# Kernel optimization log

Hardware: AMD Instinct MI355X
Metric: run time of the kernel (lower is better)

## Reference

```python
import jax, jax.numpy as jnp
import numpy as np

N, E, G, D = 100000, 1600000, 1000, 32
EPS = 1e-5


def setup_inputs() -> dict:
    key = jax.random.key(0)
    ks = jax.random.split(key, 24)
    inp = {
        'h': jax.random.normal(ks[0], (N, D), dtype=jnp.float32),
        'src': jax.random.randint(ks[1], (E,), 0, N, dtype=jnp.int32),
        'dst': jax.random.randint(ks[2], (E,), 0, N, dtype=jnp.int32),
        'graph_id': jnp.sort(jax.random.randint(ks[3], (N,), 0, G, dtype=jnp.int32)),
    }
    dims = [D, 32, 32, 32, 1]
    ki = 4
    for i in range(4):
        inp[f'conv_w{i}'] = jax.random.normal(ks[ki], (dims[i], dims[i + 1]), dtype=jnp.float32) * 0.1; ki += 1
        inp[f'conv_b{i}'] = jax.random.normal(ks[ki], (dims[i + 1],), dtype=jnp.float32) * 0.1; ki += 1
        inp[f'bn_g{i}'] = jnp.ones((dims[i + 1],), dtype=jnp.float32)
        inp[f'bn_b{i}'] = jnp.zeros((dims[i + 1],), dtype=jnp.float32)
    mlp_dims = [D + 32 + 32 + 32 + 1, 128, 64, 1]  # 129 -> 128 -> 64 -> 1
    for i in range(3):
        inp[f'mlp_w{i}'] = jax.random.normal(ks[ki], (mlp_dims[i], mlp_dims[i + 1]), dtype=jnp.float32) * 0.1; ki += 1
        inp[f'mlp_b{i}'] = jax.random.normal(ks[ki], (mlp_dims[i + 1],), dtype=jnp.float32) * 0.1; ki += 1
    return inp


def _mean_agg(x, src, dst):
    # DGL update_all(copy_u, mean): h'_v = mean of h_u over in-neighbors u of v
    deg = jax.ops.segment_sum(jnp.ones((src.shape[0],), x.dtype), dst, num_segments=N)
    agg = jax.ops.segment_sum(x[src], dst, num_segments=N)
    return agg / jnp.maximum(deg, 1.0)[:, None]


def _bn(x, g, b):
    # BatchNorm1d in training mode: batch statistics over node dim
    m = x.mean(axis=0)
    v = x.var(axis=0)
    return g * (x - m) * jax.lax.rsqrt(v + EPS) + b


def reference(h, src, dst, graph_id,
              conv_w0, conv_b0, conv_w1, conv_b1, conv_w2, conv_b2, conv_w3, conv_b3,
              bn_g0, bn_b0, bn_g1, bn_b1, bn_g2, bn_b2, bn_g3, bn_b3,
              mlp_w0, mlp_b0, mlp_w1, mlp_b1, mlp_w2, mlp_b2):
    conv = [(conv_w0, conv_b0), (conv_w1, conv_b1), (conv_w2, conv_b2), (conv_w3, conv_b3)]
    bn = [(bn_g0, bn_b0), (bn_g1, bn_b1), (bn_g2, bn_b2), (bn_g3, bn_b3)]
    h_list = [h]
    x = h
    for (w, b), (g, bb) in zip(conv, bn):
        x = _mean_agg(x, src, dst) @ w + b      # GCNConv
        x = jax.nn.relu(_bn(x, g, bb))           # BN + ReLU
        h_list.append(x)
    h_final = jnp.concatenate(h_list, axis=1)    # [N, 129]
    # dgl.mean_nodes: per-graph mean pool
    cnt = jax.ops.segment_sum(jnp.ones((N,), h_final.dtype), graph_id, num_segments=G)
    hg = jax.ops.segment_sum(h_final, graph_id, num_segments=G) / jnp.maximum(cnt, 1.0)[:, None]
    hg = jax.nn.relu(hg @ mlp_w0 + mlp_b0)
    hg = jax.nn.relu(hg @ mlp_w1 + mlp_b1)
    hg = hg @ mlp_w2 + mlp_b2
    return hg.reshape(-1)                         # [G]
```

## Files before the change

### kernel.cpp

```cpp
#include <hip/hip_runtime.h>

#define NSLOT 32
#define BN_EPS 1e-5f
#define NSB 256
#define BKBITS 8
#define BKN 256
#define MAXBUCK 512

static inline int cdiv_h(int a, int b) { return (a + b - 1) / b; }

__device__ __forceinline__ float4 f4add(float4 a, float4 b) {
    return make_float4(a.x + b.x, a.y + b.y, a.z + b.z, a.w + b.w);
}

__device__ __forceinline__ unsigned bf16rtn(float x) {
    unsigned u = __float_as_uint(x);
    return (u + 0x7FFFu + ((u >> 16) & 1u)) >> 16;
}
__device__ __forceinline__ unsigned bf16pack2(float lo, float hi) {
    return bf16rtn(lo) | (bf16rtn(hi) << 16);
}
__device__ __forceinline__ float bfLO(unsigned u) { return __uint_as_float(u << 16); }
__device__ __forceinline__ float bfHI(unsigned u) { return __uint_as_float(u & 0xFFFF0000u); }

__device__ __forceinline__ int blk_excl_scan256(int v, int t) {
    __shared__ int wsum[4];
    int l = t & 63, w = t >> 6;
    int incl = v;
#pragma unroll
    for (int off = 1; off < 64; off <<= 1) {
        int o = __shfl_up(incl, off, 64);
        if (l >= off) incl += o;
    }
    if (l == 63) wsum[w] = incl;
    __syncthreads();
    int wofs = 0;
#pragma unroll
    for (int i = 0; i < 4; i++) wofs += (i < w) ? wsum[i] : 0;
    __syncthreads();
    return wofs + incl - v;
}

__device__ __forceinline__ int blk_excl_scan512(int v, int t) {
    __shared__ int wsum8[8];
    int l = t & 63, w = t >> 6;
    int incl = v;
#pragma unroll
    for (int off = 1; off < 64; off <<= 1) {
        int o = __shfl_up(incl, off, 64);
        if (l >= off) incl += o;
    }
    if (l == 63) wsum8[w] = incl;
    __syncthreads();
    int wofs = 0;
#pragma unroll
    for (int i = 0; i < 8; i++) wofs += (i < w) ? wsum8[i] : 0;
    __syncthreads();
    return wofs + incl - v;
}

__device__ __forceinline__ void bn_coef(const float* __restrict__ sSum, const float* __restrict__ sSq,
                                        const float* __restrict__ bg, const float* __restrict__ bb,
                                        float invN, int ch, float* aOut, float* cOut) {
    float S = 0.f, Q = 0.f;
#pragma unroll
    for (int s = 0; s < NSLOT; s++) { S += sSum[s * 32 + ch]; Q += sSq[s * 32 + ch]; }
    float m = S * invN;
    float var = Q * invN - m * m;
    if (var < 0.f) var = 0.f;
    float iv = rsqrtf(var + BN_EPS);
    float a = bg[ch] * iv;
    *aOut = a;
    *cOut = bb[ch] - m * a;
}


__global__ __launch_bounds__(256) void k_hist(const int* __restrict__ dst, int* __restrict__ histT,
                                              float* __restrict__ sSum, float* __restrict__ sSq,
                                              int E, int nbuck, int chunk) {
    __shared__ int bins[MAXBUCK];
    int k = blockIdx.x, t = threadIdx.x;
    if (k == 0) {
        for (int i = t; i < 4 * NSLOT * 32; i += 256) { sSum[i] = 0.f; sSq[i] = 0.f; }
    }
    for (int b = t; b < nbuck; b += 256) bins[b] = 0;
    __syncthreads();
    int lo = k * chunk, hi = lo + chunk; if (hi > E) hi = E;
    for (int i = lo + t; i < hi; i += 256) atomicAdd(&bins[dst[i] >> BKBITS], 1);
    __syncthreads();
    for (int b = t; b < nbuck; b += 256) histT[k * nbuck + b] = bins[b];
}


__global__ __launch_bounds__(256) void k_scanA(const int* __restrict__ histT, int* __restrict__ prefixB,
                                               int* __restrict__ totalP, int* __restrict__ totalU,
                                               const int* __restrict__ gid, int* __restrict__ gstart,
                                               int nbuck, int N, int G) {
    int b = blockIdx.x, k = threadIdx.x;
    int i = b * 256 + k;
    if (i < N) {
        int g = gid[i];
        int gp = (i == 0) ? -1 : gid[i - 1];
        for (int x = gp + 1; x <= g; ++x) gstart[x] = i;
        if (i == N - 1) { for (int x = g + 1; x <= G; ++x) gstart[x] = N; }
    }
    int c = histT[k * nbuck + b];
    int pad = (c + 15) & ~15;
    int ep = blk_excl_scan256(pad, k);
    prefixB[b * NSB + k] = ep;
    int ec = blk_excl_scan256(c, k);
    if (k == NSB - 1) { totalP[b] = ep + pad; totalU[b] = ec + c; }
}

__global__ __launch_bounds__(512) void k_scanB(const int* __restrict__ totalP, const int* __restrict__ totalU,
                                               int* __restrict__ baseP, int* __restrict__ baseU, int nbuck) {
    int t = threadIdx.x;
    int vp = (t < nbuck) ? totalP[t] : 0;
    int vu = (t < nbuck) ? totalU[t] : 0;
    int ep = blk_excl_scan512(vp, t);
    int eu = blk_excl_scan512(vu, t);
    if (t < nbuck) { baseP[t] = ep; baseU[t] = eu; }
}


__global__ __launch_bounds__(256) void k_scatter2(const int* __restrict__ src, const int* __restrict__ dst,
                                                  const int* __restrict__ baseP, const int* __restrict__ prefixB,
                                                  unsigned* __restrict__ ebuf, int E, int nbuck, int chunk) {
    __shared__ int cur[MAXBUCK];
    int k = blockIdx.x, t = threadIdx.x;
    for (int b = t; b < nbuck; b += 256) cur[b] = baseP[b] + prefixB[b * NSB + k];
    __syncthreads();
    int lo = k * chunk, hi = lo + chunk; if (hi > E) hi = E;
    for (int i = lo + t; i < hi; i += 256) {
        int d = dst[i], s = src[i];
        int b = d >> BKBITS;
        int pos = atomicAdd(&cur[b], 1);
        ebuf[pos] = ((unsigned)(d & (BKN - 1)) << 24) | (unsigned)s;
    }
}


__global__ __launch_bounds__(256) void k_sortb(const unsigned* __restrict__ ebuf, const int* __restrict__ histT,
                                               const int* __restrict__ baseP, const int* __restrict__ prefixB,
                                               const int* __restrict__ baseU,
                                               int* __restrict__ col, int* __restrict__ rs, int* __restrict__ re,
                                               int nbuck, int N) {
    __shared__ int binCnt[BKN], binStart[BKN], cursor[BKN];
    __shared__ int cellBase[NSB], cellCnt[NSB];
    int b = blockIdx.x, t = threadIdx.x;
    cellBase[t] = baseP[b] + prefixB[b * NSB + t];
    cellCnt[t]  = histT[t * nbuck + b];
    binCnt[t] = 0; cursor[t] = 0;
    __syncthreads();
    {
        int cb = cellBase[t], cc = cellCnt[t];
        for (int j = 0; j < cc; j++) atomicAdd(&binCnt[ebuf[cb + j] >> 24], 1);
    }
    __syncthreads();
    int bs = blk_excl_scan256(binCnt[t], t);
    binStart[t] = bs;
    __syncthreads();
    int colBase = baseU[b];
    {
        int cb = cellBase[t], cc = cellCnt[t];
        for (int j = 0; j < cc; j++) {
            unsigned e = ebuf[cb + j];
            int l = e >> 24;
            int pos = binStart[l] + atomicAdd(&cursor[l], 1);
            col[colBase + pos] = (int)(e & 0xFFFFFFu);
        }
    }
    int node = b * BKN + t;
    if (node < N) {
        rs[node] = colBase + binStart[t];
        re[node] = colBase + binStart[t] + binCnt[t];
    }
}


template <int AFF>
__global__ __launch_bounds__(256) void k_transform(const void* __restrict__ xin, const float* __restrict__ W,
                                                   const float* __restrict__ sSum, const float* __restrict__ sSq,
                                                   const float* __restrict__ bg, const float* __restrict__ bb,
                                                   uint4* __restrict__ pb, int n, float invN) {
    __shared__ float sW[32][32];
    __shared__ float sA[32], sC[32];
    int t = threadIdx.x;
    for (int i = t; i < 1024; i += 256) sW[i >> 5][i & 31] = W[i];
    if (AFF && t < 32) bn_coef(sSum, sSq, bg, bb, invN, t, &sA[t], &sC[t]);
    __syncthreads();
    int node = blockIdx.x * 256 + t;
    if (node >= n) return;
    float x[32];
    if (AFF) {
        const uint4* y4 = (const uint4*)xin + (size_t)node * 4;
#pragma unroll
        for (int q = 0; q < 4; q++) {
            uint4 u = y4[q];
            x[8*q+0] = bfLO(u.x); x[8*q+1] = bfHI(u.x);
            x[8*q+2] = bfLO(u.y); x[8*q+3] = bfHI(u.y);
            x[8*q+4] = bfLO(u.z); x[8*q+5] = bfHI(u.z);
            x[8*q+6] = bfLO(u.w); x[8*q+7] = bfHI(u.w);
        }
#pragma unroll
        for (int k = 0; k < 32; k++) {
            float v = sA[k] * x[k] + sC[k];
            x[k] = v > 0.f ? v : 0.f;
        }
    } else {
        const float4* s4 = (const float4*)xin + (size_t)node * 8;
#pragma unroll
        for (int q = 0; q < 8; q++) {
            float4 v = s4[q];
            x[4*q] = v.x; x[4*q+1] = v.y; x[4*q+2] = v.z; x[4*q+3] = v.w;
        }
    }
    float acc[32];
#pragma unroll
    for (int f = 0; f < 32; f++) acc[f] = 0.f;
#pragma unroll
    for (int k = 0; k < 32; k++) {
        float xv = x[k];
#pragma unroll
        for (int f = 0; f < 32; f++) acc[f] += xv * sW[k][f];
    }
    uint4* d4 = pb + (size_t)node * 4;
#pragma unroll
    for (int q = 0; q < 4; q++) {
        uint4 o;
        o.x = bf16pack2(acc[8*q+0], acc[8*q+1]);
        o.y = bf16pack2(acc[8*q+2], acc[8*q+3]);
        o.z = bf16pack2(acc[8*q+4], acc[8*q+5]);
        o.w = bf16pack2(acc[8*q+6], acc[8*q+7]);
        d4[q] = o;
    }
}

__global__ __launch_bounds__(256) void k_transform3(const uint4* __restrict__ y2, const float* __restrict__ w3,
                                                    const float* __restrict__ sSum, const float* __restrict__ sSq,
                                                    const float* __restrict__ bg, const float* __restrict__ bb,
                                                    float* __restrict__ p3, int n, float invN) {
    __shared__ float sw[32], sA[32], sC[32];
    int t = threadIdx.x;
    if (t < 32) { sw[t] = w3[t]; bn_coef(sSum, sSq, bg, bb, invN, t, &sA[t], &sC[t]); }
    __syncthreads();
    int i = blockIdx.x * 256 + t;
    if (i >= n) return;
    const uint4* x4 = y2 + (size_t)i * 4;
    float acc = 0.f;
#pragma unroll
    for (int q = 0; q < 4; q++) {
        uint4 u = x4[q];
        float vv[8] = { bfLO(u.x), bfHI(u.x), bfLO(u.y), bfHI(u.y),
                        bfLO(u.z), bfHI(u.z), bfLO(u.w), bfHI(u.w) };
#pragma unroll
        for (int r = 0; r < 8; r++) {
            int k = q * 8 + r;
            float xv = sA[k] * vv[r] + sC[k];
            xv = xv > 0.f ? xv : 0.f;
            acc += xv * sw[k];
        }
    }
    p3[i] = acc;
}


__global__ __launch_bounds__(256) void k_aggregate(const uint4* __restrict__ pb, const int* __restrict__ rs,
                                                   const int* __restrict__ re, const int* __restrict__ col,
                                                   const float* __restrict__ bias,
                                                   uint4* __restrict__ yb, float* __restrict__ sSum,
                                                   float* __restrict__ sSq, int n) {
    __shared__ int scol[2048];
    int t = threadIdx.x;
    int lane = t & 3;
    int grp = t >> 2;
    int node0 = blockIdx.x * 64;
    int node = node0 + grp;
    int base0 = 0, len = 0;
    if (node0 < n) {
        int last = node0 + 63; if (last > n - 1) last = n - 1;
        base0 = rs[node0];
        len = re[last] - base0;
    }
    bool lds = (len > 0 && len <= 2048);
    if (lds) { for (int i = t; i < len; i += 256) scol[i] = col[base0 + i]; }
    __syncthreads();

    float accA[8], accB[8];
#pragma unroll
    for (int q = 0; q < 8; q++) { accA[q] = 0.f; accB[q] = 0.f; }
    float vout[8];
#pragma unroll
    for (int q = 0; q < 8; q++) vout[q] = 0.f;
    if (node < n) {
        int s0 = rs[node], s1 = re[node];
#define GATH(vv, c) uint4 vv = pb[(size_t)(c) * 4 + lane]
#define ACC(dst, vv) \
        dst[0] += bfLO((vv).x); dst[1] += bfHI((vv).x); \
        dst[2] += bfLO((vv).y); dst[3] += bfHI((vv).y); \
        dst[4] += bfLO((vv).z); dst[5] += bfHI((vv).z); \
        dst[6] += bfLO((vv).w); dst[7] += bfHI((vv).w)
        if (lds) {
            int j = s0 - base0, j1 = s1 - base0;
            for (; j + 8 <= j1; j += 8) {
                int c0 = scol[j], c1 = scol[j + 1], c2 = scol[j + 2], c3 = scol[j + 3];
                int c4 = scol[j + 4], c5 = scol[j + 5], c6 = scol[j + 6], c7 = scol[j + 7];
                GATH(g0, c0); GATH(g1, c1); GATH(g2, c2); GATH(g3, c3);
                GATH(g4, c4); GATH(g5, c5); GATH(g6, c6); GATH(g7, c7);
                ACC(accA, g0); ACC(accB, g1); ACC(accA, g2); ACC(accB, g3);
                ACC(accA, g4); ACC(accB, g5); ACC(accA, g6); ACC(accB, g7);
            }
            for (; j < j1; ++j) { GATH(g, scol[j]); ACC(accA, g); }
        } else {
            for (int j = s0; j < s1; ++j) { GATH(g, col[j]); ACC(accA, g); }
        }
#undef GATH
#undef ACC
        int deg = s1 - s0;
        float inv = (deg > 0) ? 1.f / (float)deg : 1.f;
        const float4* b4 = (const float4*)bias;
        float4 b0 = b4[lane * 2], b1 = b4[lane * 2 + 1];
        vout[0] = (accA[0] + accB[0]) * inv + b0.x;
        vout[1] = (accA[1] + accB[1]) * inv + b0.y;
        vout[2] = (accA[2] + accB[2]) * inv + b0.z;
        vout[3] = (accA[3] + accB[3]) * inv + b0.w;
        vout[4] = (accA[4] + accB[4]) * inv + b1.x;
        vout[5] = (accA[5] + accB[5]) * inv + b1.y;
        vout[6] = (accA[6] + accB[6]) * inv + b1.z;
        vout[7] = (accA[7] + accB[7]) * inv + b1.w;
        uint4 o;
        o.x = bf16pack2(vout[0], vout[1]);
        o.y = bf16pack2(vout[2], vout[3]);
        o.z = bf16pack2(vout[4], vout[5]);
        o.w = bf16pack2(vout[6], vout[7]);
        yb[(size_t)node * 4 + lane] = o;
    }
    __shared__ float sS[64][32];
    __shared__ float sQ[64][32];
    ((float4*)&sS[grp][lane * 8])[0] = make_float4(vout[0], vout[1], vout[2], vout[3]);
    ((float4*)&sS[grp][lane * 8])[1] = make_float4(vout[4], vout[5], vout[6], vout[7]);
    ((float4*)&sQ[grp][lane * 8])[0] = make_float4(vout[0]*vout[0], vout[1]*vout[1], vout[2]*vout[2], vout[3]*vout[3]);
    ((float4*)&sQ[grp][lane * 8])[1] = make_float4(vout[4]*vout[4], vout[5]*vout[5], vout[6]*vout[6], vout[7]*vout[7]);
    __syncthreads();
    if (t < 32) {
        float S = 0.f, Q = 0.f;
#pragma unroll
        for (int g2 = 0; g2 < 64; g2++) { S += sS[g2][t]; Q += sQ[g2][t]; }
        int slot = blockIdx.x & (NSLOT - 1);
        atomicAdd(&sSum[slot * 32 + t], S);
        atomicAdd(&sSq[slot * 32 + t], Q);
    }
}

__global__ __launch_bounds__(256) void k_aggregate3(const float* __restrict__ p3, const int* __restrict__ rs,
                                                    const int* __restrict__ re, const int* __restrict__ col,
                                                    const float* __restrict__ b1,
                                                    float* __restrict__ y3, float* __restrict__ sSum,
                                                    float* __restrict__ sSq, int n) {
    int i = blockIdx.x * 256 + threadIdx.x;
    float lsum = 0.f, lsq = 0.f;
    if (i < n) {
        int s0 = rs[i], s1 = re[i];
        float a0 = 0.f, a1 = 0.f, a2 = 0.f, a3 = 0.f;
        int j = s0;
        for (; j + 4 <= s1; j += 4) {
            int c0 = col[j], c1 = col[j + 1], c2 = col[j + 2], c3 = col[j + 3];
            a0 += p3[c0]; a1 += p3[c1]; a2 += p3[c2]; a3 += p3[c3];
        }
        for (; j < s1; ++j) a0 += p3[col[j]];
        float acc = (a0 + a1) + (a2 + a3);
        float inv = (s1 > s0) ? 1.f / (float)(s1 - s0) : 1.f;
        float v = acc * inv + b1[0];
        y3[i] = v; lsum = v; lsq = v * v;
    }
    __shared__ float sS[256], sQ[256];
    int t = threadIdx.x;
    sS[t] = lsum; sQ[t] = lsq;
    __syncthreads();
    for (int s = 128; s > 0; s >>= 1) {
        if (t < s) { sS[t] += sS[t + s]; sQ[t] += sQ[t + s]; }
        __syncthreads();
    }
    if (t == 0) {
        int slot = blockIdx.x & (NSLOT - 1);
        atomicAdd(&sSum[slot * 32], sS[0]);
        atomicAdd(&sSq[slot * 32], sQ[0]);
    }
}


__global__ __launch_bounds__(256) void k_pool_mlp(const float* __restrict__ h,
                                                  const unsigned* __restrict__ y0b,
                                                  const unsigned* __restrict__ y1b,
                                                  const unsigned* __restrict__ y2b,
                                                  const float* __restrict__ y3,
                                                  const float* __restrict__ sSum, const float* __restrict__ sSq,
                                                  const float* __restrict__ bg0, const float* __restrict__ bb0,
                                                  const float* __restrict__ bg1, const float* __restrict__ bb1,
                                                  const float* __restrict__ bg2, const float* __restrict__ bb2,
                                                  const float* __restrict__ bg3, const float* __restrict__ bb3,
                                                  const int* __restrict__ gstart,
                                                  const float* __restrict__ w0, const float* __restrict__ b0,
                                                  const float* __restrict__ w1, const float* __restrict__ b1,
                                                  const float* __restrict__ w2, const float* __restrict__ b2,
                                                  float* __restrict__ out, float invN) {
    __shared__ float pcA[128], pcC[128];
    int g = blockIdx.x;
    int t = threadIdx.x;
    if (t < 97) {
        int layer = (t == 96) ? 3 : (t >> 5);
        int ch = t & 31;
        const float* bg = (layer == 0) ? bg0 : (layer == 1) ? bg1 : (layer == 2) ? bg2 : bg3;
        const float* bb = (layer == 0) ? bb0 : (layer == 1) ? bb1 : (layer == 2) ? bb2 : bb3;
        bn_coef(sSum + layer * NSLOT * 32, sSq + layer * NSLOT * 32, bg, bb, invN, ch, &pcA[t], &pcC[t]);
    }
    __syncthreads();
    int s0 = gstart[g], s1 = gstart[g + 1];
    int lane = t & 31, slot = t >> 5;
    int arr = lane >> 3, sub = lane & 7;
    const unsigned* yb = (arr == 1) ? y0b : (arr == 2) ? y1b : y2b;
    float4 a4 = make_float4(1.f, 1.f, 1.f, 1.f);
    float4 c4 = make_float4(0.f, 0.f, 0.f, 0.f);
    bool aff = (arr > 0);
    if (aff) {
        a4 = ((const float4*)pcA)[(arr - 1) * 8 + sub];
        c4 = ((const float4*)pcC)[(arr - 1) * 8 + sub];
    }
    float4 acc = make_float4(0.f, 0.f, 0.f, 0.f);
    for (int n = s0 + slot; n < s1; n += 8) {
        float4 v;
        if (arr == 0) {
            v = ((const float4*)h)[(size_t)n * 8 + sub];
        } else {
            uint2 u = ((const uint2*)yb)[(size_t)n * 8 + sub];
            v = make_float4(bfLO(u.x), bfHI(u.x), bfLO(u.y), bfHI(u.y));
        }
        if (aff) {
            float vx = fmaf(a4.x, v.x, c4.x); vx = vx > 0.f ? vx : 0.f;
            float vy = fmaf(a4.y, v.y, c4.y); vy = vy > 0.f ? vy : 0.f;
            float vz = fmaf(a4.z, v.z, c4.z); vz = vz > 0.f ? vz : 0.f;
            float vw = fmaf(a4.w, v.w, c4.w); vw = vw > 0.f ? vw : 0.f;
            v = make_float4(vx, vy, vz, vw);
        }
        acc = f4add(acc, v);
    }
    __shared__ float sP[8][128];
    __shared__ float sY[8];
    ((float4*)&sP[slot][lane * 4])[0] = acc;
    if (t < 8) {
        float a = pcA[96], c = pcC[96], s = 0.f;
        for (int n = s0 + t; n < s1; n += 8) {
            float v = fmaf(a, y3[n], c);
            s += v > 0.f ? v : 0.f;
        }
        sY[t] = s;
    }
    __syncthreads();
    __shared__ float hg[129];
    __shared__ float hid1[128];
    __shared__ float hid2[64];
    float inv = (s1 > s0) ? 1.f / (float)(s1 - s0) : 1.f;
    if (t < 128) {
        float S = 0.f;
#pragma unroll
        for (int s = 0; s < 8; s++) S += sP[s][t];
        hg[t] = S * inv;
    } else if (t == 128) {
        float S = 0.f;
#pragma unroll
        for (int s = 0; s < 8; s++) S += sY[s];
        hg[128] = S * inv;
    }
    __syncthreads();
    if (t < 128) {
        float a = b0[t];
        for (int i = 0; i < 129; i++) a += hg[i] * w0[i * 128 + t];
        hid1[t] = a > 0.f ? a : 0.f;
    }
    __syncthreads();
    if (t < 64) {
        float a = b1[t];
        for (int i = 0; i < 128; i++) a += hid1[i] * w1[i * 64 + t];
        hid2[t] = a > 0.f ? a : 0.f;
    }
    __syncthreads();
    if (t < 64) {
        float v = hid2[t] * w2[t];
        for (int off = 32; off > 0; off >>= 1) v += __shfl_down(v, off, 64);
        if (t == 0) out[g] = v + b2[0];
    }
}


extern "C" void kernel_launch(void* const* d_in, const int* in_sizes, int n_in,
                              void* d_out, int out_size, void* d_ws, size_t ws_size,
                              hipStream_t stream) {
    const float* h   = (const float*)d_in[0];
    const int* src   = (const int*)d_in[1];
    const int* dst   = (const int*)d_in[2];
    const int* gid   = (const int*)d_in[3];
    const float* convw[4], *convb[4], *bng[4], *bnb[4];
    for (int i = 0; i < 4; i++) {
        convw[i] = (const float*)d_in[4 + 4 * i];
        convb[i] = (const float*)d_in[5 + 4 * i];
        bng[i]   = (const float*)d_in[6 + 4 * i];
        bnb[i]   = (const float*)d_in[7 + 4 * i];
    }
    const float* mw0 = (const float*)d_in[20];
    const float* mb0 = (const float*)d_in[21];
    const float* mw1 = (const float*)d_in[22];
    const float* mb1 = (const float*)d_in[23];
    const float* mw2 = (const float*)d_in[24];
    const float* mb2 = (const float*)d_in[25];

    const int N = in_sizes[0] / 32;
    const int E = in_sizes[1];
    const int G = out_size;
    const int nbuck = cdiv_h(N, BKN);
    const int chunk = cdiv_h(E, NSB);

    char* ws = (char*)d_ws;
    size_t off = 0;
    auto alloc = [&](size_t bytes) -> void* {
        void* p = ws + off;
        off += (bytes + 511) & ~(size_t)511;
        return p;
    };
    int* histT   = (int*)alloc((size_t)NSB * nbuck * 4);
    int* prefixB = (int*)alloc((size_t)nbuck * NSB * 4);
    int* totalP  = (int*)alloc((size_t)nbuck * 4);
    int* totalU  = (int*)alloc((size_t)nbuck * 4);
    int* basePp  = (int*)alloc((size_t)nbuck * 4);
    int* baseUp  = (int*)alloc((size_t)nbuck * 4);
    size_t ebufE = (size_t)E + (size_t)16 * NSB * nbuck;
    size_t ovl   = ebufE * 4;
    size_t pB    = (size_t)N * 64;
    if (pB > ovl) ovl = pB;
    unsigned* ebuf = (unsigned*)alloc(ovl);
    uint4* pb    = (uint4*)ebuf;
    int* col     = (int*)alloc((size_t)E * 4);
    int* rs      = (int*)alloc((size_t)N * 4);
    int* re      = (int*)alloc((size_t)N * 4);
    int* gstart  = (int*)alloc((size_t)(G + 1) * 4);
    uint4* y0b   = (uint4*)alloc((size_t)N * 64);
    uint4* y1b   = (uint4*)alloc((size_t)N * 64);
    uint4* y2b   = (uint4*)alloc((size_t)N * 64);
    float* y3    = (float*)alloc((size_t)N * 4);
    float* sSum  = (float*)alloc((size_t)4 * NSLOT * 32 * 4);
    float* sSq   = (float*)alloc((size_t)4 * NSLOT * 32 * 4);
    (void)ws_size; (void)n_in;

    const int NB_N = cdiv_h(N, 256);
    const int NB_AG = cdiv_h(N, 64);
    const float invN = 1.f / (float)N;

    k_hist<<<NSB, 256, 0, stream>>>(dst, histT, sSum, sSq, E, nbuck, chunk);
    k_scanA<<<nbuck, 256, 0, stream>>>(histT, prefixB, totalP, totalU, gid, gstart, nbuck, N, G);
    k_scanB<<<1, 512, 0, stream>>>(totalP, totalU, basePp, baseUp, nbuck);
    k_scatter2<<<NSB, 256, 0, stream>>>(src, dst, basePp, prefixB, ebuf, E, nbuck, chunk);
    k_sortb<<<nbuck, 256, 0, stream>>>(ebuf, histT, basePp, prefixB, baseUp, col, rs, re, nbuck, N);

    k_transform<0><<<NB_N, 256, 0, stream>>>(h, convw[0], nullptr, nullptr, nullptr, nullptr, pb, N, invN);
    k_aggregate<<<NB_AG, 256, 0, stream>>>(pb, rs, re, col, convb[0], y0b,
                                           sSum + 0 * NSLOT * 32, sSq + 0 * NSLOT * 32, N);
    k_transform<1><<<NB_N, 256, 0, stream>>>(y0b, convw[1], sSum + 0 * NSLOT * 32, sSq + 0 * NSLOT * 32,
                                             bng[0], bnb[0], pb, N, invN);
    k_aggregate<<<NB_AG, 256, 0, stream>>>(pb, rs, re, col, convb[1], y1b,
                                           sSum + 1 * NSLOT * 32, sSq + 1 * NSLOT * 32, N);
    k_transform<1><<<NB_N, 256, 0, stream>>>(y1b, convw[2], sSum + 1 * NSLOT * 32, sSq + 1 * NSLOT * 32,
                                             bng[1], bnb[1], pb, N, invN);
    k_aggregate<<<NB_AG, 256, 0, stream>>>(pb, rs, re, col, convb[2], y2b,
                                           sSum + 2 * NSLOT * 32, sSq + 2 * NSLOT * 32, N);
    k_transform3<<<NB_N, 256, 0, stream>>>(y2b, convw[3], sSum + 2 * NSLOT * 32, sSq + 2 * NSLOT * 32,
                                           bng[2], bnb[2], (float*)pb, N, invN);
    k_aggregate3<<<NB_N, 256, 0, stream>>>((float*)pb, rs, re, col, convb[3], y3,
                                           sSum + 3 * NSLOT * 32, sSq + 3 * NSLOT * 32, N);

    k_pool_mlp<<<G, 256, 0, stream>>>(h, (const unsigned*)y0b, (const unsigned*)y1b, (const unsigned*)y2b,
                                      y3, sSum, sSq,
                                      bng[0], bnb[0], bng[1], bnb[1], bng[2], bnb[2], bng[3], bnb[3],
                                      gstart, mw0, mb0, mw1, mb1, mw2, mb2, (float*)d_out, invN);
}
```

Baseline: 317.5 us.

## Use wave shuffles for BN reductions, shrink gather unroll, raise occupancy

k_aggregate now requests 8 blocks per CU through launch_bounds and halves the gather unroll from 8 to 4 to lower register pressure. Its BN statistic reduction now uses wave-level xor shuffles instead of a 64x32 shared-memory tree, which frees LDS. k_aggregate3 also switches its block reduction to shuffles, and k_pool_mlp spreads the per-graph y3 pooling over all 256 threads instead of 8. The trade-off is that fewer independent gather loads are in flight per thread, and the extra shuffle work may offset the occupancy gain.

```diff
diff --git a/kernel.cpp b/kernel.cpp
--- a/kernel.cpp
+++ b/kernel.cpp
@@ -265,12 +265,14 @@
 }
 
 
-__global__ __launch_bounds__(256) void k_aggregate(const uint4* __restrict__ pb, const int* __restrict__ rs,
-                                                   const int* __restrict__ re, const int* __restrict__ col,
-                                                   const float* __restrict__ bias,
-                                                   uint4* __restrict__ yb, float* __restrict__ sSum,
-                                                   float* __restrict__ sSq, int n) {
+__global__ __launch_bounds__(256, 8) void k_aggregate(const uint4* __restrict__ pb, const int* __restrict__ rs,
+                                                      const int* __restrict__ re, const int* __restrict__ col,
+                                                      const float* __restrict__ bias,
+                                                      uint4* __restrict__ yb, float* __restrict__ sSum,
+                                                      float* __restrict__ sSq, int n) {
     __shared__ int scol[2048];
+    __shared__ float sWS[4][32];
+    __shared__ float sWQ[4][32];
     int t = threadIdx.x;
     int lane = t & 3;
     int grp = t >> 2;
@@ -302,17 +304,20 @@
         dst[6] += bfLO((vv).w); dst[7] += bfHI((vv).w)
         if (lds) {
             int j = s0 - base0, j1 = s1 - base0;
-            for (; j + 8 <= j1; j += 8) {
+            for (; j + 4 <= j1; j += 4) {
                 int c0 = scol[j], c1 = scol[j + 1], c2 = scol[j + 2], c3 = scol[j + 3];
-                int c4 = scol[j + 4], c5 = scol[j + 5], c6 = scol[j + 6], c7 = scol[j + 7];
                 GATH(g0, c0); GATH(g1, c1); GATH(g2, c2); GATH(g3, c3);
-                GATH(g4, c4); GATH(g5, c5); GATH(g6, c6); GATH(g7, c7);
                 ACC(accA, g0); ACC(accB, g1); ACC(accA, g2); ACC(accB, g3);
-                ACC(accA, g4); ACC(accB, g5); ACC(accA, g6); ACC(accB, g7);
             }
             for (; j < j1; ++j) { GATH(g, scol[j]); ACC(accA, g); }
         } else {
-            for (int j = s0; j < s1; ++j) { GATH(g, col[j]); ACC(accA, g); }
+            int j = s0;
+            for (; j + 4 <= s1; j += 4) {
+                int c0 = col[j], c1 = col[j + 1], c2 = col[j + 2], c3 = col[j + 3];
+                GATH(g0, c0); GATH(g1, c1); GATH(g2, c2); GATH(g3, c3);
+                ACC(accA, g0); ACC(accB, g1); ACC(accA, g2); ACC(accB, g3);
+            }
+            for (; j < s1; ++j) { GATH(g, col[j]); ACC(accA, g); }
         }
 #undef GATH
 #undef ACC
@@ -335,17 +340,26 @@
         o.w = bf16pack2(vout[6], vout[7]);
         yb[(size_t)node * 4 + lane] = o;
     }
-    __shared__ float sS[64][32];
-    __shared__ float sQ[64][32];
-    ((float4*)&sS[grp][lane * 8])[0] = make_float4(vout[0], vout[1], vout[2], vout[3]);
-    ((float4*)&sS[grp][lane * 8])[1] = make_float4(vout[4], vout[5], vout[6], vout[7]);
-    ((float4*)&sQ[grp][lane * 8])[0] = make_float4(vout[0]*vout[0], vout[1]*vout[1], vout[2]*vout[2], vout[3]*vout[3]);
-    ((float4*)&sQ[grp][lane * 8])[1] = make_float4(vout[4]*vout[4], vout[5]*vout[5], vout[6]*vout[6], vout[7]*vout[7]);
+    float sqv[8];
+#pragma unroll
+    for (int q = 0; q < 8; q++) sqv[q] = vout[q] * vout[q];
+#pragma unroll
+    for (int off = 4; off < 64; off <<= 1) {
+#pragma unroll
+        for (int q = 0; q < 8; q++) {
+            vout[q] += __shfl_xor(vout[q], off, 64);
+            sqv[q]  += __shfl_xor(sqv[q],  off, 64);
+        }
+    }
+    int w = t >> 6, l = t & 63;
+    if (l < 4) {
+#pragma unroll
+        for (int q = 0; q < 8; q++) { sWS[w][l * 8 + q] = vout[q]; sWQ[w][l * 8 + q] = sqv[q]; }
+    }
     __syncthreads();
     if (t < 32) {
-        float S = 0.f, Q = 0.f;
-#pragma unroll
-        for (int g2 = 0; g2 < 64; g2++) { S += sS[g2][t]; Q += sQ[g2][t]; }
+        float S = sWS[0][t] + sWS[1][t] + sWS[2][t] + sWS[3][t];
+        float Q = sWQ[0][t] + sWQ[1][t] + sWQ[2][t] + sWQ[3][t];
         int slot = blockIdx.x & (NSLOT - 1);
         atomicAdd(&sSum[slot * 32 + t], S);
         atomicAdd(&sSq[slot * 32 + t], Q);
@@ -357,7 +371,8 @@
                                                     const float* __restrict__ b1,
                                                     float* __restrict__ y3, float* __restrict__ sSum,
                                                     float* __restrict__ sSq, int n) {
-    int i = blockIdx.x * 256 + threadIdx.x;
+    int t = threadIdx.x;
+    int i = blockIdx.x * 256 + t;
     float lsum = 0.f, lsq = 0.f;
     if (i < n) {
         int s0 = rs[i], s1 = re[i];
@@ -373,18 +388,20 @@
         float v = acc * inv + b1[0];
         y3[i] = v; lsum = v; lsq = v * v;
     }
-    __shared__ float sS[256], sQ[256];
-    int t = threadIdx.x;
-    sS[t] = lsum; sQ[t] = lsq;
-    __syncthreads();
-    for (int s = 128; s > 0; s >>= 1) {
-        if (t < s) { sS[t] += sS[t + s]; sQ[t] += sQ[t + s]; }
-        __syncthreads();
-    }
+#pragma unroll
+    for (int off = 1; off < 64; off <<= 1) {
+        lsum += __shfl_xor(lsum, off, 64);
+        lsq  += __shfl_xor(lsq,  off, 64);
+    }
+    __shared__ float sWS3[4], sWQ3[4];
+    if ((t & 63) == 0) { sWS3[t >> 6] = lsum; sWQ3[t >> 6] = lsq; }
+    __syncthreads();
     if (t == 0) {
+        float S = sWS3[0] + sWS3[1] + sWS3[2] + sWS3[3];
+        float Q = sWQ3[0] + sWQ3[1] + sWQ3[2] + sWQ3[3];
         int slot = blockIdx.x & (NSLOT - 1);
-        atomicAdd(&sSum[slot * 32], sS[0]);
-        atomicAdd(&sSq[slot * 32], sQ[0]);
+        atomicAdd(&sSum[slot * 32], S);
+        atomicAdd(&sSq[slot * 32], Q);
     }
 }
 
@@ -444,17 +461,20 @@
         }
         acc = f4add(acc, v);
     }
+    float ys = 0.f;
+    {
+        float a = pcA[96], c = pcC[96];
+        for (int n = s0 + t; n < s1; n += 256) {
+            float v = fmaf(a, y3[n], c);
+            ys += v > 0.f ? v : 0.f;
+        }
+    }
+#pragma unroll
+    for (int off = 1; off < 64; off <<= 1) ys += __shfl_xor(ys, off, 64);
     __shared__ float sP[8][128];
-    __shared__ float sY[8];
+    __shared__ float sY[4];
+    if ((t & 63) == 0) sY[t >> 6] = ys;
     ((float4*)&sP[slot][lane * 4])[0] = acc;
-    if (t < 8) {
-        float a = pcA[96], c = pcC[96], s = 0.f;
-        for (int n = s0 + t; n < s1; n += 8) {
-            float v = fmaf(a, y3[n], c);
-            s += v > 0.f ? v : 0.f;
-        }
-        sY[t] = s;
-    }
     __syncthreads();
     __shared__ float hg[129];
     __shared__ float hid1[128];
@@ -466,9 +486,7 @@
         for (int s = 0; s < 8; s++) S += sP[s][t];
         hg[t] = S * inv;
     } else if (t == 128) {
-        float S = 0.f;
-#pragma unroll
-        for (int s = 0; s < 8; s++) S += sY[s];
+        float S = sY[0] + sY[1] + sY[2] + sY[3];
         hg[128] = S * inv;
     }
     __syncthreads();
```

Result: faster. 304.7 us (-4.0%).
